# Kernel tuning notes

Hardware: AMD Instinct MI355X
Metric: run time of the kernel (lower is better)

The kernel has to match this reference:

```python
import jax, jax.numpy as jnp
import numpy as np
from math import sqrt, pi

EMBED, HEADS, ATTN, MLP = 1024, 16, 1024, 4096
HEAD_DIM = ATTN // HEADS
EPS = 1e-5

def _ln(x):
    mu = jnp.mean(x, axis=-1, keepdims=True)
    var = jnp.var(x, axis=-1, keepdims=True)
    return (x - mu) / jnp.sqrt(var + EPS)

def _gelu(x):
    return 0.5 * x * (1.0 + jnp.tanh(sqrt(2.0 / pi) * (x + 0.044715 * x**3)))

def setup_inputs() -> dict:
    key = jax.random.key(0)
    ks = jax.random.split(key, 6)
    B, S = 2, 2048
    x = jax.random.normal(ks[0], (B, S, EMBED), dtype=jnp.float32)
    # weights stored as [in, out] (transpose of torch's [out, in]); math identical
    w_qkv = jax.random.normal(ks[1], (EMBED, 3 * ATTN), dtype=jnp.float32) / sqrt(EMBED)
    w_fc = jax.random.normal(ks[2], (ATTN, EMBED), dtype=jnp.float32) / sqrt(ATTN)
    w1 = jax.random.normal(ks[3], (EMBED, MLP), dtype=jnp.float32) / sqrt(EMBED)
    b1 = jnp.zeros((MLP,), dtype=jnp.float32)
    w2 = jax.random.normal(ks[4], (MLP, EMBED), dtype=jnp.float32) / sqrt(MLP)
    b2 = jnp.zeros((EMBED,), dtype=jnp.float32)
    return {"x": x, "w_qkv": w_qkv, "w_fc": w_fc, "w1": w1, "b1": b1, "w2": w2, "b2": b2}

def reference(x, w_qkv, w_fc, w1, b1, w2, b2):
    B, S, _ = x.shape
    res = x
    h = _ln(x)
    qkv = h @ w_qkv                                   # [B,S,3*ATTN]
    q, k, v = jnp.split(qkv, 3, axis=-1)
    q = q.reshape(B, S, HEADS, HEAD_DIM)
    k = k.reshape(B, S, HEADS, HEAD_DIM)
    v = v.reshape(B, S, HEADS, HEAD_DIM)
    attn = jnp.einsum('bqnc,bknc->bnqk', q, k) / sqrt(HEAD_DIM)  # [B,H,S,S]
    attn = jax.nn.softmax(attn, axis=-1)
    attn_val = jnp.einsum('bnqk,bknc->bqnc', attn, v).reshape(B, S, ATTN)
    x = res + attn_val @ w_fc
    res = x
    h = _ln(x)
    h = _gelu(h @ w1 + b1) @ w2 + b2
    return res + h
```

## Files before the change

kernel.cpp:

```cpp
#include <hip/hip_runtime.h>

typedef unsigned short u16;
typedef __attribute__((ext_vector_type(8))) short bf16x8;
typedef __attribute__((ext_vector_type(4))) short s16x4;
typedef __attribute__((ext_vector_type(4))) float f32x4;

#define DEV __device__ __forceinline__

DEV u16 f2bf(float f) {
  union { float f; unsigned u; } v; v.f = f;
  unsigned r = v.u + 0x7fffu + ((v.u >> 16) & 1u);
  return (u16)(r >> 16);
}
DEV u16 f2bf_tr(float f) {
  union { float f; unsigned u; } v; v.f = f;
  return (u16)(v.u >> 16);
}

DEV int swzi(int row, int col) { return row * 64 + (col ^ ((row & 7) << 3)); }

DEV void gl16(const u16* g, u16* l) {
  __builtin_amdgcn_global_load_lds((const __attribute__((address_space(1))) void*)g,
                                   (__attribute__((address_space(3))) void*)l, 16, 0, 0);
}

template <int N> DEV void waitv() {
  asm volatile("s_waitcnt vmcnt(%0)" :: "n"(N) : "memory");
}

__global__ __launch_bounds__(256) void wcastT(const float* __restrict__ w,
                                              u16* __restrict__ wt, int K, int N) {
  __shared__ float t[32][33];
  int n0 = blockIdx.x * 32, k0 = blockIdx.y * 32;
  int tx = threadIdx.x & 31, ty = threadIdx.x >> 5;
#pragma unroll
  for (int i = 0; i < 32; i += 8)
    t[ty + i][tx] = w[(size_t)(k0 + ty + i) * N + n0 + tx];
  __syncthreads();
#pragma unroll
  for (int i = 0; i < 32; i += 8)
    wt[(size_t)(n0 + ty + i) * K + k0 + tx] = f2bf(t[tx][ty + i]);
}

__global__ __launch_bounds__(256) void vtransp(const u16* __restrict__ v,
                                               u16* __restrict__ vt) {
  __shared__ u16 t[32][34];
  int s0 = blockIdx.x * 32, d0 = blockIdx.y * 32;
  int bh = blockIdx.z; int b = bh >> 4, h = bh & 15;
  int tx = threadIdx.x & 31, ty = threadIdx.x >> 5;
#pragma unroll
  for (int i = 0; i < 32; i += 8)
    t[ty + i][tx] = v[(size_t)(b * 2048 + s0 + ty + i) * 1024 + h * 64 + d0 + tx];
  __syncthreads();
#pragma unroll
  for (int i = 0; i < 32; i += 8)
    vt[((size_t)(b * 16 + h) * 64 + d0 + ty + i) * 2048 + s0 + tx] = t[tx][ty + i];
}

__global__ __launch_bounds__(256) void ln_kernel(const float* __restrict__ x,
                                                 u16* __restrict__ out) {
  int row = blockIdx.x, tid = threadIdx.x;
  const float4* xr = (const float4*)(x + (size_t)row * 1024);
  float4 f = xr[tid];
  float s = f.x + f.y + f.z + f.w;
  float s2 = f.x * f.x + f.y * f.y + f.z * f.z + f.w * f.w;
#pragma unroll
  for (int o = 1; o < 64; o <<= 1) { s += __shfl_xor(s, o); s2 += __shfl_xor(s2, o); }
  __shared__ float red[2][4];
  int wid = tid >> 6;
  if ((tid & 63) == 0) { red[0][wid] = s; red[1][wid] = s2; }
  __syncthreads();
  float tot  = red[0][0] + red[0][1] + red[0][2] + red[0][3];
  float tot2 = red[1][0] + red[1][1] + red[1][2] + red[1][3];
  float mu = tot * (1.0f / 1024.0f);
  float var = tot2 * (1.0f / 1024.0f) - mu * mu;
  float rstd = rsqrtf(var + 1e-5f);
  s16x4 o4;
  o4[0] = (short)f2bf((f.x - mu) * rstd);
  o4[1] = (short)f2bf((f.y - mu) * rstd);
  o4[2] = (short)f2bf((f.z - mu) * rstd);
  o4[3] = (short)f2bf((f.w - mu) * rstd);
  *(s16x4*)(out + (size_t)row * 1024 + tid * 4) = o4;
}

template <int MODE, int BM, int BK>
__global__ __launch_bounds__(256) void gemm_bt(
    const u16* __restrict__ A, const u16* __restrict__ Bt, int N, int K,
    const float* __restrict__ resid, const float* __restrict__ bias,
    float* __restrict__ outF, u16* __restrict__ o0, u16* __restrict__ o1,
    u16* __restrict__ o2) {
  constexpr int MR = BM / 32;
  constexpr int KH = BK / 32;
  constexpr int LDEPTH = KH * (BM / 64 + 2);
  constexpr int ACH = BM * 32, BCH = 128 * 32;
  __shared__ __align__(16) u16 lA[2 * KH * ACH];
  __shared__ __align__(16) u16 lB[2 * KH * BCH];
  int tid = threadIdx.x;
  int lane = tid & 63, wid = tid >> 6;
  int lr = lane & 15, lg = lane >> 4;

  int gx = gridDim.x;
  int nwg = gx * gridDim.y;
  int bid = blockIdx.y * gx + blockIdx.x;
  int swz = (bid & 7) * (nwg >> 3) + (bid >> 3);
  int rowBase = (swz / gx) * BM, colBase = (swz % gx) * 128;
  int wr = (wid >> 1) * (MR * 16), wc = (wid & 1) * 64;

  int srow = wid * 16 + (lane >> 2);
  int scol = (lane & 3) * 8;
  const u16* gA = A + (size_t)(rowBase + srow) * K + scol;
  const u16* gB = Bt + (size_t)(colBase + srow) * K + scol;
  u16* lAb = &lA[wid * 16 * 32];
  u16* lBb = &lB[wid * 16 * 32];

  auto stage = [&](int t, int buf) {
    int k0 = t * BK;
#pragma unroll
    for (int kk = 0; kk < KH; kk++) {
      u16* dA = lAb + buf * KH * ACH + kk * ACH;
      u16* dB = lBb + buf * KH * BCH + kk * BCH;
      int koff = k0 + kk * 32;
#pragma unroll
      for (int c = 0; c < BM / 64; c++)
        gl16(gA + (size_t)c * 64 * K + koff, dA + c * 64 * 32);
#pragma unroll
      for (int c = 0; c < 2; c++)
        gl16(gB + (size_t)c * 64 * K + koff, dB + c * 64 * 32);
    }
  };

  f32x4 acc[MR][4];
  f32x4 zero = {0.f, 0.f, 0.f, 0.f};
#pragma unroll
  for (int m = 0; m < MR; m++)
#pragma unroll
    for (int n = 0; n < 4; n++) acc[m][n] = zero;

  stage(0, 0);

  int nt = K / BK;
  for (int t = 0; t < nt; t++) {
    int cur = t & 1;
    if (t + 1 < nt) {
      stage(t + 1, cur ^ 1);
      waitv<LDEPTH>();
    } else {
      waitv<0>();
    }
    __builtin_amdgcn_s_barrier();
    asm volatile("" ::: "memory");

    const u16* cA = &lA[cur * KH * ACH];
    const u16* cB = &lB[cur * KH * BCH];
#pragma unroll
    for (int kk = 0; kk < KH; kk++) {
      bf16x8 af[MR], bfv[4];
#pragma unroll
      for (int m = 0; m < MR; m++)
        af[m] = *(const bf16x8*)&cA[kk * ACH + (wr + m * 16 + lr) * 32 + lg * 8];
#pragma unroll
      for (int n = 0; n < 4; n++)
        bfv[n] = *(const bf16x8*)&cB[kk * BCH + (wc + n * 16 + lr) * 32 + lg * 8];
#pragma unroll
      for (int m = 0; m < MR; m++)
#pragma unroll
        for (int n = 0; n < 4; n++)
          acc[m][n] = __builtin_amdgcn_mfma_f32_16x16x32_bf16(bfv[n], af[m], acc[m][n], 0, 0, 0);
    }

    asm volatile("" ::: "memory");
    __builtin_amdgcn_s_barrier();
  }

#pragma unroll
  for (int m = 0; m < MR; m++) {
    int grow = rowBase + wr + m * 16 + lr;
#pragma unroll
    for (int n = 0; n < 4; n++) {
      int gcol = colBase + wc + n * 16 + lg * 4;
      f32x4 v4 = acc[m][n];
      if constexpr (MODE == 0) {
        bool isq = gcol < 1024;
        u16* dst = isq ? o0 : ((gcol < 2048) ? o1 : o2);
        s16x4 o4;
#pragma unroll
        for (int j = 0; j < 4; j++)
          o4[j] = (short)f2bf(isq ? v4[j] * 0.18033688011112042f : v4[j]);
        *(s16x4*)&dst[(size_t)grow * 1024 + (gcol & 1023)] = o4;
      } else if constexpr (MODE == 1) {
        size_t idx = (size_t)grow * N + gcol;
        float4 r = *(const float4*)&resid[idx];
        float4 ov = {r.x + v4[0], r.y + v4[1], r.z + v4[2], r.w + v4[3]};
        *(float4*)&outF[idx] = ov;
      } else if constexpr (MODE == 2) {
        float4 bq = *(const float4*)&bias[gcol];
        s16x4 o4;
#pragma unroll
        for (int j = 0; j < 4; j++) {
          float g = v4[j] + ((const float*)&bq)[j];
          float e = __builtin_amdgcn_exp2f(2.302208198f * (g + 0.044715f * g * g * g));
          o4[j] = (short)f2bf(g - g * __builtin_amdgcn_rcpf(1.0f + e));
        }
        *(s16x4*)&o0[(size_t)grow * N + gcol] = o4;
      } else {
        size_t idx = (size_t)grow * N + gcol;
        float4 r = *(const float4*)&resid[idx];
        float4 bq = *(const float4*)&bias[gcol];
        float4 ov = {r.x + bq.x + v4[0], r.y + bq.y + v4[1],
                     r.z + bq.z + v4[2], r.w + bq.w + v4[3]};
        *(float4*)&outF[idx] = ov;
      }
    }
  }
}

__global__ __launch_bounds__(256) void attn_kernel(const u16* __restrict__ q,
                                                   const u16* __restrict__ k,
                                                   const u16* __restrict__ vt,
                                                   u16* __restrict__ o) {
  __shared__ __align__(16) u16 lK[64 * 64];
  __shared__ __align__(16) u16 lV[64 * 64];
  __shared__ __align__(16) u16 lP[4 * 16 * 64];
  const int S = 2048, E = 1024;
  int qt = blockIdx.x, h = blockIdx.y, b = blockIdx.z;
  int tid = threadIdx.x, wid = tid >> 6, lane = tid & 63;
  int lr = lane & 15, lg = lane >> 4;
  u16* lPw = &lP[wid * 1024];

  const u16* qp = q + ((size_t)b * S + qt * 64 + wid * 16) * E + h * 64;
  const u16* kp = k + (size_t)b * S * E + h * 64;
  const u16* vp = vt + ((size_t)(b * 16 + h) * 64) * S;

  bf16x8 aQ[2];
#pragma unroll
  for (int kk = 0; kk < 2; kk++)
    aQ[kk] = *(const bf16x8*)(qp + (size_t)lr * E + kk * 32 + lg * 8);

  bf16x8 onesv;
#pragma unroll
  for (int i = 0; i < 8; i++) onesv[i] = (short)0x3F80;

  f32x4 accO[4], accL;
  float Mx = -1e30f;
  f32x4 zero = {0.f, 0.f, 0.f, 0.f};
  accL = zero;
#pragma unroll
  for (int nn = 0; nn < 4; nn++) accO[nn] = zero;

  int sr_ = tid >> 3, sc_ = (tid & 7) * 8;
  const u16* kps0 = kp + (size_t)sr_ * E + sc_;
  const u16* kps1 = kp + (size_t)(sr_ + 32) * E + sc_;
  const u16* vps0 = vp + (size_t)sr_ * S + sc_;
  const u16* vps1 = vp + (size_t)(sr_ + 32) * S + sc_;

  bf16x8 rk0 = *(const bf16x8*)(kps0);
  bf16x8 rk1 = *(const bf16x8*)(kps1);
  bf16x8 rv0 = *(const bf16x8*)(vps0);
  bf16x8 rv1 = *(const bf16x8*)(vps1);

  for (int kv0 = 0; kv0 < S; kv0 += 64) {
    __syncthreads();
    *(bf16x8*)&lK[swzi(sr_, sc_)] = rk0;
    *(bf16x8*)&lK[swzi(32 + sr_, sc_)] = rk1;
    *(bf16x8*)&lV[swzi(sr_, sc_)] = rv0;
    *(bf16x8*)&lV[swzi(32 + sr_, sc_)] = rv1;
    int nx = kv0 + 64;
    if (nx < S) {
      rk0 = *(const bf16x8*)(kps0 + (size_t)nx * E);
      rk1 = *(const bf16x8*)(kps1 + (size_t)nx * E);
      rv0 = *(const bf16x8*)(vps0 + nx);
      rv1 = *(const bf16x8*)(vps1 + nx);
    }
    __syncthreads();

    f32x4 sc4[4];
#pragma unroll
    for (int n = 0; n < 4; n++) sc4[n] = zero;
#pragma unroll
    for (int n = 0; n < 4; n++) {
      bf16x8 bk0 = *(const bf16x8*)&lK[swzi(n * 16 + lr, lg * 8)];
      bf16x8 bk1 = *(const bf16x8*)&lK[swzi(n * 16 + lr, 32 + lg * 8)];
      sc4[n] = __builtin_amdgcn_mfma_f32_16x16x32_bf16(bk0, aQ[0], sc4[n], 0, 0, 0);
      sc4[n] = __builtin_amdgcn_mfma_f32_16x16x32_bf16(bk1, aQ[1], sc4[n], 0, 0, 0);
    }

    float a0 = fmaxf(fmaxf(sc4[0][0], sc4[0][1]), fmaxf(sc4[0][2], sc4[0][3]));
    float a1 = fmaxf(fmaxf(sc4[1][0], sc4[1][1]), fmaxf(sc4[1][2], sc4[1][3]));
    float a2 = fmaxf(fmaxf(sc4[2][0], sc4[2][1]), fmaxf(sc4[2][2], sc4[2][3]));
    float a3 = fmaxf(fmaxf(sc4[3][0], sc4[3][1]), fmaxf(sc4[3][2], sc4[3][3]));
    float mxr = fmaxf(fmaxf(a0, a1), fmaxf(a2, a3));
    mxr = fmaxf(mxr, __shfl_xor(mxr, 16));
    mxr = fmaxf(mxr, __shfl_xor(mxr, 32));
    if (__any(mxr > Mx + 8.f)) {
      float nm = fmaxf(Mx, mxr);
      float s = __builtin_amdgcn_exp2f(Mx - nm);
      Mx = nm;
      accL *= s;
#pragma unroll
      for (int nn = 0; nn < 4; nn++) accO[nn] *= s;
    }
#pragma unroll
    for (int n = 0; n < 4; n++) {
      s16x4 pq;
#pragma unroll
      for (int j = 0; j < 4; j++)
        pq[j] = (short)f2bf_tr(__builtin_amdgcn_exp2f(sc4[n][j] - Mx));
      *(s16x4*)&lPw[swzi(lr, n * 16 + lg * 4)] = pq;
    }

#pragma unroll
    for (int kk = 0; kk < 2; kk++) {
      bf16x8 ap = *(const bf16x8*)&lPw[swzi(lr, kk * 32 + lg * 8)];
      accL = __builtin_amdgcn_mfma_f32_16x16x32_bf16(onesv, ap, accL, 0, 0, 0);
#pragma unroll
      for (int nn = 0; nn < 4; nn++) {
        bf16x8 bv = *(const bf16x8*)&lV[swzi(nn * 16 + lr, kk * 32 + lg * 8)];
        accO[nn] = __builtin_amdgcn_mfma_f32_16x16x32_bf16(bv, ap, accO[nn], 0, 0, 0);
      }
    }
  }

  float inv = __builtin_amdgcn_rcpf(accL[0]);
  int srow = qt * 64 + wid * 16 + lr;
#pragma unroll
  for (int nn = 0; nn < 4; nn++) {
    s16x4 o4;
#pragma unroll
    for (int j = 0; j < 4; j++) o4[j] = (short)f2bf(accO[nn][j] * inv);
    *(s16x4*)&o[((size_t)b * S + srow) * E + h * 64 + nn * 16 + lg * 4] = o4;
  }
}

extern "C" void kernel_launch(void* const* d_in, const int* in_sizes, int n_in,
                              void* d_out, int out_size, void* d_ws, size_t ws_size,
                              hipStream_t stream) {
  (void)in_sizes; (void)n_in; (void)out_size; (void)ws_size;
  const float* x     = (const float*)d_in[0];
  const float* w_qkv = (const float*)d_in[1];
  const float* w_fc  = (const float*)d_in[2];
  const float* w1    = (const float*)d_in[3];
  const float* b1    = (const float*)d_in[4];
  const float* w2    = (const float*)d_in[5];
  const float* b2    = (const float*)d_in[6];
  float* out = (float*)d_out;
  char* ws = (char*)d_ws;

  u16* wqkvT = (u16*)(ws);
  u16* wfcT  = (u16*)(ws + 6291456);
  u16* w1T   = (u16*)(ws + 8388608);
  u16* w2T   = (u16*)(ws + 16777216);
  u16* hbuf  = (u16*)(ws + 25165824);
  u16* qbuf  = (u16*)(ws + 33554432);
  u16* kbuf  = (u16*)(ws + 41943040);
  u16* vbuf  = (u16*)(ws + 50331648);
  u16* vtbuf = (u16*)(ws + 58720256);
  float* x2  = (float*)(ws + 67108864);
  u16* act   = qbuf;

  wcastT<<<dim3(96, 32), 256, 0, stream>>>(w_qkv, wqkvT, 1024, 3072);
  wcastT<<<dim3(32, 32), 256, 0, stream>>>(w_fc, wfcT, 1024, 1024);
  wcastT<<<dim3(128, 32), 256, 0, stream>>>(w1, w1T, 1024, 4096);
  wcastT<<<dim3(32, 128), 256, 0, stream>>>(w2, w2T, 4096, 1024);

  ln_kernel<<<4096, 256, 0, stream>>>(x, hbuf);
  gemm_bt<0, 128, 32><<<dim3(24, 32), 256, 0, stream>>>(hbuf, wqkvT, 3072, 1024,
                                                        nullptr, nullptr, nullptr,
                                                        qbuf, kbuf, vbuf);
  vtransp<<<dim3(64, 2, 32), 256, 0, stream>>>(vbuf, vtbuf);
  attn_kernel<<<dim3(32, 16, 2), 256, 0, stream>>>(qbuf, kbuf, vtbuf, hbuf);
  gemm_bt<1, 64, 64><<<dim3(8, 64), 256, 0, stream>>>(hbuf, wfcT, 1024, 1024,
                                                      x, nullptr, x2,
                                                      nullptr, nullptr, nullptr);
  ln_kernel<<<4096, 256, 0, stream>>>(x2, hbuf);
  gemm_bt<2, 128, 32><<<dim3(32, 32), 256, 0, stream>>>(hbuf, w1T, 4096, 1024,
                                                        nullptr, b1, nullptr,
                                                        act, nullptr, nullptr);
  gemm_bt<3, 64, 64><<<dim3(8, 64), 256, 0, stream>>>(act, w2T, 1024, 4096,
                                                      x2, b2, out,
                                                      nullptr, nullptr, nullptr);
}
```

Before: 264.1 us.

## Rewrite attention with 32x32x16 MFMA, register-resident P, and 128-row query tiles

The attention kernel moves from 16x16x32 to 32x32x16 bf16 MFMA. Each wave now handles 32 query rows, so a block covers 128 rows and the grid is halved. The probabilities stay in registers and are repacked into the PV operand with cross-half shuffles, which removes the per-wave LDS staging of P. The row sum is now a plain register reduction instead of an MFMA against a ones vector. This cuts LDS traffic and reuses each K/V tile across twice as many queries, but raises register pressure and leaves only 512 blocks.

Result: no change. 266.7 us (+1.0%).

```diff
diff --git a/kernel.cpp b/kernel.cpp
--- a/kernel.cpp
+++ b/kernel.cpp
@@ -4,6 +4,8 @@
 typedef __attribute__((ext_vector_type(8))) short bf16x8;
 typedef __attribute__((ext_vector_type(4))) short s16x4;
 typedef __attribute__((ext_vector_type(4))) float f32x4;
+typedef __attribute__((ext_vector_type(16))) float f32x16;
+typedef __attribute__((ext_vector_type(4))) int i32x4;
 
 #define DEV __device__ __forceinline__
 
@@ -12,9 +14,9 @@
   unsigned r = v.u + 0x7fffu + ((v.u >> 16) & 1u);
   return (u16)(r >> 16);
 }
-DEV u16 f2bf_tr(float f) {
-  union { float f; unsigned u; } v; v.f = f;
-  return (u16)(v.u >> 16);
+DEV int packbf(float a, float b) {
+  union { float f; unsigned u; } x, y; x.f = a; y.f = b;
+  return (int)((y.u & 0xFFFF0000u) | (x.u >> 16));
 }
 
 DEV int swzi(int row, int col) { return row * 64 + (col ^ ((row & 7) << 3)); }
@@ -220,32 +222,26 @@
                                                    u16* __restrict__ o) {
   __shared__ __align__(16) u16 lK[64 * 64];
   __shared__ __align__(16) u16 lV[64 * 64];
-  __shared__ __align__(16) u16 lP[4 * 16 * 64];
   const int S = 2048, E = 1024;
   int qt = blockIdx.x, h = blockIdx.y, b = blockIdx.z;
   int tid = threadIdx.x, wid = tid >> 6, lane = tid & 63;
-  int lr = lane & 15, lg = lane >> 4;
-  u16* lPw = &lP[wid * 1024];
-
-  const u16* qp = q + ((size_t)b * S + qt * 64 + wid * 16) * E + h * 64;
+  int l31 = lane & 31, hi = lane >> 5;
+
+  const u16* qp = q + ((size_t)b * S + qt * 128 + wid * 32) * E + h * 64;
   const u16* kp = k + (size_t)b * S * E + h * 64;
   const u16* vp = vt + ((size_t)(b * 16 + h) * 64) * S;
 
-  bf16x8 aQ[2];
-#pragma unroll
-  for (int kk = 0; kk < 2; kk++)
-    aQ[kk] = *(const bf16x8*)(qp + (size_t)lr * E + kk * 32 + lg * 8);
-
-  bf16x8 onesv;
-#pragma unroll
-  for (int i = 0; i < 8; i++) onesv[i] = (short)0x3F80;
-
-  f32x4 accO[4], accL;
-  float Mx = -1e30f;
-  f32x4 zero = {0.f, 0.f, 0.f, 0.f};
-  accL = zero;
-#pragma unroll
-  for (int nn = 0; nn < 4; nn++) accO[nn] = zero;
+  bf16x8 aQ[4];
+#pragma unroll
+  for (int s = 0; s < 4; s++)
+    aQ[s] = *(const bf16x8*)(qp + (size_t)l31 * E + s * 16 + hi * 8);
+
+  f32x16 accO[2];
+  float accL = 0.f, Mx = -1e30f;
+#pragma unroll
+  for (int dh = 0; dh < 2; dh++)
+#pragma unroll
+    for (int r = 0; r < 16; r++) accO[dh][r] = 0.f;
 
   int sr_ = tid >> 3, sc_ = (tid & 7) * 8;
   const u16* kps0 = kp + (size_t)sr_ * E + sc_;
@@ -273,62 +269,80 @@
     }
     __syncthreads();
 
-    f32x4 sc4[4];
-#pragma unroll
-    for (int n = 0; n < 4; n++) sc4[n] = zero;
-#pragma unroll
-    for (int n = 0; n < 4; n++) {
-      bf16x8 bk0 = *(const bf16x8*)&lK[swzi(n * 16 + lr, lg * 8)];
-      bf16x8 bk1 = *(const bf16x8*)&lK[swzi(n * 16 + lr, 32 + lg * 8)];
-      sc4[n] = __builtin_amdgcn_mfma_f32_16x16x32_bf16(bk0, aQ[0], sc4[n], 0, 0, 0);
-      sc4[n] = __builtin_amdgcn_mfma_f32_16x16x32_bf16(bk1, aQ[1], sc4[n], 0, 0, 0);
-    }
-
-    float a0 = fmaxf(fmaxf(sc4[0][0], sc4[0][1]), fmaxf(sc4[0][2], sc4[0][3]));
-    float a1 = fmaxf(fmaxf(sc4[1][0], sc4[1][1]), fmaxf(sc4[1][2], sc4[1][3]));
-    float a2 = fmaxf(fmaxf(sc4[2][0], sc4[2][1]), fmaxf(sc4[2][2], sc4[2][3]));
-    float a3 = fmaxf(fmaxf(sc4[3][0], sc4[3][1]), fmaxf(sc4[3][2], sc4[3][3]));
-    float mxr = fmaxf(fmaxf(a0, a1), fmaxf(a2, a3));
-    mxr = fmaxf(mxr, __shfl_xor(mxr, 16));
-    mxr = fmaxf(mxr, __shfl_xor(mxr, 32));
-    if (__any(mxr > Mx + 8.f)) {
-      float nm = fmaxf(Mx, mxr);
-      float s = __builtin_amdgcn_exp2f(Mx - nm);
-      Mx = nm;
-      accL *= s;
-#pragma unroll
-      for (int nn = 0; nn < 4; nn++) accO[nn] *= s;
-    }
-#pragma unroll
-    for (int n = 0; n < 4; n++) {
-      s16x4 pq;
-#pragma unroll
-      for (int j = 0; j < 4; j++)
-        pq[j] = (short)f2bf_tr(__builtin_amdgcn_exp2f(sc4[n][j] - Mx));
-      *(s16x4*)&lPw[swzi(lr, n * 16 + lg * 4)] = pq;
-    }
-
-#pragma unroll
-    for (int kk = 0; kk < 2; kk++) {
-      bf16x8 ap = *(const bf16x8*)&lPw[swzi(lr, kk * 32 + lg * 8)];
-      accL = __builtin_amdgcn_mfma_f32_16x16x32_bf16(onesv, ap, accL, 0, 0, 0);
-#pragma unroll
-      for (int nn = 0; nn < 4; nn++) {
-        bf16x8 bv = *(const bf16x8*)&lV[swzi(nn * 16 + lr, kk * 32 + lg * 8)];
-        accO[nn] = __builtin_amdgcn_mfma_f32_16x16x32_bf16(bv, ap, accO[nn], 0, 0, 0);
+    f32x16 sc[2];
+#pragma unroll
+    for (int kvh = 0; kvh < 2; kvh++)
+#pragma unroll
+      for (int r = 0; r < 16; r++) sc[kvh][r] = 0.f;
+#pragma unroll
+    for (int kvh = 0; kvh < 2; kvh++)
+#pragma unroll
+      for (int s = 0; s < 4; s++) {
+        bf16x8 kf = *(const bf16x8*)&lK[swzi(l31 + kvh * 32, s * 16 + hi * 8)];
+        sc[kvh] = __builtin_amdgcn_mfma_f32_32x32x16_bf16(kf, aQ[s], sc[kvh], 0, 0, 0);
       }
+
+    float mx = sc[0][0];
+#pragma unroll
+    for (int r = 1; r < 16; r++) mx = fmaxf(mx, sc[0][r]);
+#pragma unroll
+    for (int r = 0; r < 16; r++) mx = fmaxf(mx, sc[1][r]);
+    mx = fmaxf(mx, __shfl_xor(mx, 32));
+    if (__any(mx > Mx + 8.f)) {
+      float nm = fmaxf(Mx, mx);
+      float sr = __builtin_amdgcn_exp2f(Mx - nm);
+      Mx = nm; accL *= sr;
+#pragma unroll
+      for (int dh = 0; dh < 2; dh++)
+#pragma unroll
+        for (int r = 0; r < 16; r++) accO[dh][r] *= sr;
+    }
+    float sum = 0.f;
+#pragma unroll
+    for (int kvh = 0; kvh < 2; kvh++)
+#pragma unroll
+      for (int r = 0; r < 16; r++) {
+        float p = __builtin_amdgcn_exp2f(sc[kvh][r] - Mx);
+        sc[kvh][r] = p; sum += p;
+      }
+    sum += __shfl_xor(sum, 32);
+    accL += sum;
+
+#pragma unroll
+    for (int kk = 0; kk < 4; kk++) {
+      int kvh = kk >> 1, r0 = (kk & 1) * 8;
+      int u0 = packbf(sc[kvh][r0 + 0], sc[kvh][r0 + 1]);
+      int u1 = packbf(sc[kvh][r0 + 2], sc[kvh][r0 + 3]);
+      int v0 = packbf(sc[kvh][r0 + 4], sc[kvh][r0 + 5]);
+      int v1 = packbf(sc[kvh][r0 + 6], sc[kvh][r0 + 7]);
+      int xu0 = __shfl_xor(u0, 32), xu1 = __shfl_xor(u1, 32);
+      int xv0 = __shfl_xor(v0, 32), xv1 = __shfl_xor(v1, 32);
+      union { i32x4 w; bf16x8 hv; } pf;
+      pf.w[0] = hi ? xv0 : u0;
+      pf.w[1] = hi ? xv1 : u1;
+      pf.w[2] = hi ? v0 : xu0;
+      pf.w[3] = hi ? v1 : xu1;
+#pragma unroll
+      for (int dh = 0; dh < 2; dh++) {
+        bf16x8 vf = *(const bf16x8*)&lV[swzi(l31 + dh * 32, kk * 16 + hi * 8)];
+        accO[dh] = __builtin_amdgcn_mfma_f32_32x32x16_bf16(vf, pf.hv, accO[dh], 0, 0, 0);
+      }
     }
   }
 
-  float inv = __builtin_amdgcn_rcpf(accL[0]);
-  int srow = qt * 64 + wid * 16 + lr;
-#pragma unroll
-  for (int nn = 0; nn < 4; nn++) {
-    s16x4 o4;
-#pragma unroll
-    for (int j = 0; j < 4; j++) o4[j] = (short)f2bf(accO[nn][j] * inv);
-    *(s16x4*)&o[((size_t)b * S + srow) * E + h * 64 + nn * 16 + lg * 4] = o4;
-  }
+  float inv = __builtin_amdgcn_rcpf(accL);
+  int srow = qt * 128 + wid * 32 + l31;
+  u16* op = o + ((size_t)b * S + srow) * E + h * 64;
+#pragma unroll
+  for (int dh = 0; dh < 2; dh++)
+#pragma unroll
+    for (int g = 0; g < 4; g++) {
+      int d = 8 * g + 4 * hi + 32 * dh;
+      s16x4 o4;
+#pragma unroll
+      for (int j = 0; j < 4; j++) o4[j] = (short)f2bf(accO[dh][4 * g + j] * inv);
+      *(s16x4*)&op[d] = o4;
+    }
 }
 
 extern "C" void kernel_launch(void* const* d_in, const int* in_sizes, int n_in,
@@ -367,7 +381,7 @@
                                                         nullptr, nullptr, nullptr,
                                                         qbuf, kbuf, vbuf);
   vtransp<<<dim3(64, 2, 32), 256, 0, stream>>>(vbuf, vtbuf);
-  attn_kernel<<<dim3(32, 16, 2), 256, 0, stream>>>(qbuf, kbuf, vtbuf, hbuf);
+  attn_kernel<<<dim3(16, 16, 2), 256, 0, stream>>>(qbuf, kbuf, vtbuf, hbuf);
   gemm_bt<1, 64, 64><<<dim3(8, 64), 256, 0, stream>>>(hbuf, wfcT, 1024, 1024,
                                                       x, nullptr, x2,
                                                       nullptr, nullptr, nullptr);
```
